# Optimization experiments

Measured on AMD Instinct MI355X. Metric: run time of the kernel, lower is better.

The kernel has to match this reference:

```python
import jax, jax.numpy as jnp
import numpy as np

D_MODEL, N_HEADS, D_HEAD = 1024, 16, 64
BATCH, SEQ = 4, 2048


def setup_inputs() -> dict:
    key = jax.random.key(0)
    ks = jax.random.split(key, 10)
    s = 1.0 / np.sqrt(D_MODEL)
    x = jax.random.normal(ks[0], (BATCH, SEQ, D_MODEL), dtype=jnp.float32)
    attention_mask = jax.random.randint(ks[1], (BATCH, SEQ), 0, 2).astype(jnp.bool_)
    # guarantee at least one attended key per batch row (avoid all -inf softmax)
    attention_mask = attention_mask.at[:, 0].set(True)
    def lin(k):
        kw, kb = jax.random.split(k)
        W = jax.random.uniform(kw, (D_MODEL, D_MODEL), jnp.float32, -s, s)
        b = jax.random.uniform(kb, (D_MODEL,), jnp.float32, -s, s)
        return W, b
    Wq, bq = lin(ks[2]); Wk, bk = lin(ks[3]); Wv, bv = lin(ks[4]); Wo, bo = lin(ks[5])
    return {"x": x, "attention_mask": attention_mask,
            "Wq": Wq, "bq": bq, "Wk": Wk, "bk": bk,
            "Wv": Wv, "bv": bv, "Wo": Wo, "bo": bo}


def reference(x, attention_mask, Wq, bq, Wk, bk, Wv, bv, Wo, bo):
    B, S, _ = x.shape
    def proj(W, b):  # [B,S,d_model] -> [B,S,H,Dh]
        return (x @ W + b).reshape(B, S, N_HEADS, D_HEAD)
    q = proj(Wq, bq)
    k = proj(Wk, bk)
    v = proj(Wv, bv)
    scores = jnp.einsum('bqhd,bkhd->bhqk', q, k)  # [B,H,S,S]
    add_mask = jnp.where(attention_mask, 0.0, jnp.inf)[:, None, None, :]
    # faithful order: subtract mask, THEN scale (inf survives division)
    probs = jax.nn.softmax((scores - add_mask) / jnp.sqrt(jnp.float32(D_HEAD)), axis=-1)
    attn = jnp.einsum('bhqk,bkhd->bqhd', probs, v).reshape(B, S, N_HEADS * D_HEAD)
    return attn @ Wo + bo
```

## Files before the change

kernel.cpp:

```cpp
#include <hip/hip_runtime.h>
#include <hip/hip_bf16.h>
#include <math.h>

#define BATCH 4
#define SEQ   2048
#define DM    1024
#define NH    16
#define DH    64
#define MROWS (BATCH * SEQ)

typedef unsigned short ushort_t;
typedef unsigned int   uint_t;
typedef __attribute__((ext_vector_type(8))) short  short8;
typedef __attribute__((ext_vector_type(4))) float  float4v;

#define QSCALE 0.1803368801111244f

__device__ __forceinline__ ushort_t f2bf(float v) {
    uint_t u = __float_as_uint(v);
    u += 0x7FFFu + ((u >> 16) & 1u);
    return (ushort_t)(u >> 16);
}
__device__ __forceinline__ float bf2f(ushort_t h) {
    return __uint_as_float(((uint_t)h) << 16);
}
__device__ __forceinline__ void gload_lds16(const ushort_t* g, ushort_t* lds) {
    __builtin_amdgcn_global_load_lds(
        (const __attribute__((address_space(1))) void*)g,
        (__attribute__((address_space(3))) void*)lds, 16, 0, 0);
}

__global__ __launch_bounds__(256) void conv_x(
    const float* __restrict__ src, ushort_t* __restrict__ dst, int n4)
{
    int i = blockIdx.x * 256 + threadIdx.x;
    if (i >= n4) return;
    float4 v = ((const float4*)src)[i];
    ((ushort4*)dst)[i] = make_ushort4(f2bf(v.x), f2bf(v.y), f2bf(v.z), f2bf(v.w));
}

__global__ __launch_bounds__(256) void convT_w4(
    const float* __restrict__ W0, const float* __restrict__ W1,
    const float* __restrict__ W2, const float* __restrict__ W3,
    ushort_t* __restrict__ fused, ushort_t* __restrict__ woh,
    ushort_t* __restrict__ wol)
{
    __shared__ float sT[64][65];
    const int z = blockIdx.z;
    const float* W = (z == 0) ? W0 : (z == 1) ? W1 : (z == 2) ? W2 : W3;
    ushort_t* ht = (z < 3) ? fused + (size_t)z * 1024 * 1024 : woh;
    const int n0 = blockIdx.x * 64, k0 = blockIdx.y * 64;
    const int t = threadIdx.x;
#pragma unroll
    for (int i = 0; i < 16; i++) {
        int idx = t + i * 256, r = idx >> 6, c = idx & 63;
        sT[r][c] = W[(size_t)(k0 + r) * 1024 + n0 + c];
    }
    __syncthreads();
#pragma unroll
    for (int i = 0; i < 16; i++) {
        int idx = t + i * 256, r = idx >> 6, c = idx & 63;
        float v = sT[c][r];
        ushort_t h = f2bf(v);
        ht[(size_t)(n0 + r) * 1024 + k0 + c] = h;
        if (z == 3) wol[(size_t)(n0 + r) * 1024 + k0 + c] = f2bf(v - bf2f(h));
    }
}

__global__ __launch_bounds__(256) void gemm_qkv(
    const ushort_t* __restrict__ A, const ushort_t* __restrict__ Bt,
    const float* __restrict__ bq, const float* __restrict__ bk,
    const float* __restrict__ bv, const int* __restrict__ mask,
    ushort_t* __restrict__ Qh, ushort_t* __restrict__ Kh,
    ushort_t* __restrict__ Vt)
{
    __shared__ __align__(16) ushort_t smem[8192];
    const int t = threadIdx.x, lane = t & 63, w = t >> 6;
    const int n0 = blockIdx.x * 128, m0 = blockIdx.y * 128;
    const int wm = (w >> 1) * 64, wn = (w & 1) * 64;
    const int lq = lane >> 4, lc = lane & 15;
    const int gl = (lane & 3) ^ ((lane >> 3) & 3);
    const int irow = lane >> 2;
    const int sect = n0 >> 10;
    const float* bsel = (sect == 0) ? bq : (sect == 1) ? bk : bv;
    const float scl = (sect == 0) ? QSCALE : 1.0f;

    float4v acc[4][4];
#pragma unroll
    for (int i = 0; i < 4; i++)
#pragma unroll
        for (int j = 0; j < 4; j++) acc[i][j] = (float4v)(0.0f);

    for (int k0 = 0; k0 < 1024; k0 += 32) {
        __syncthreads();
#pragma unroll
        for (int j = 0; j < 4; j++) {
            const int i = w * 4 + j;
            const ushort_t* src = (i < 8)
                ? A  + (size_t)(m0 + i * 16 + irow) * 1024 + k0 + gl * 8
                : Bt + (size_t)(n0 + (i - 8) * 16 + irow) * 1024 + k0 + gl * 8;
            gload_lds16(src, &smem[i * 512]);
        }
        __syncthreads();

        short8 av[4], bvf[4];
#pragma unroll
        for (int mt = 0; mt < 4; mt++) {
            const int r = wm + mt * 16 + lc;
            av[mt] = *(const short8*)&smem[r * 32 + ((lq ^ ((r >> 1) & 3)) * 8)];
        }
#pragma unroll
        for (int nt = 0; nt < 4; nt++) {
            const int r = wn + nt * 16 + lc;
            bvf[nt] = *(const short8*)&smem[4096 + r * 32 + ((lq ^ ((r >> 1) & 3)) * 8)];
        }
#pragma unroll
        for (int nt = 0; nt < 4; nt++)
#pragma unroll
            for (int mt = 0; mt < 4; mt++)
                acc[mt][nt] = __builtin_amdgcn_mfma_f32_16x16x32_bf16(av[mt], bvf[nt], acc[mt][nt], 0, 0, 0);
    }

#pragma unroll
    for (int nt = 0; nt < 4; nt++) {
        const int nn = (n0 + wn + nt * 16 + lc) & 1023;
        const float bvv = bsel[nn];
        const int h = nn >> 6, d = nn & 63;
#pragma unroll
        for (int mt = 0; mt < 4; mt++) {
            const int mbase = m0 + wm + mt * 16 + lq * 4;
            const int b = mbase >> 11, s0 = mbase & 2047;
            int mk[4] = {1, 1, 1, 1};
            if (sect != 0) {
                const int4 m4 = *(const int4*)&mask[b * 2048 + s0];
                mk[0] = m4.x; mk[1] = m4.y; mk[2] = m4.z; mk[3] = m4.w;
            }
            if (sect == 2) {
                ushort_t hh[4];
#pragma unroll
                for (int r = 0; r < 4; r++)
                    hh[r] = mk[r] ? f2bf(acc[mt][nt][r] + bvv) : (ushort_t)0;
                *(ushort4*)&Vt[((size_t)(b * 16 + h) * 64 + d) * 2048 + s0] =
                    make_ushort4(hh[0], hh[1], hh[2], hh[3]);
            } else {
                ushort_t* dst = (sect == 0) ? Qh : Kh;
#pragma unroll
                for (int r = 0; r < 4; r++)
                    dst[((size_t)(b * 16 + h) * 2048 + s0 + r) * 64 + d] =
                        mk[r] ? f2bf((acc[mt][nt][r] + bvv) * scl) : (ushort_t)0;
            }
        }
    }
}

__global__ __launch_bounds__(256) void gemm_split3(
    const ushort_t* __restrict__ Ah, const ushort_t* __restrict__ Al,
    const ushort_t* __restrict__ Bh, const ushort_t* __restrict__ Bl,
    const float* __restrict__ bias, float* __restrict__ out)
{
    __shared__ __align__(16) ushort_t smem[16384];
    const int t = threadIdx.x, lane = t & 63, w = t >> 6;
    const int n0 = blockIdx.x * 128, m0 = blockIdx.y * 128;
    const int wm = (w >> 1) * 64, wn = (w & 1) * 64;
    const int lq = lane >> 4, lc = lane & 15;
    const int gl = (lane & 3) ^ ((lane >> 3) & 3);
    const int irow = lane >> 2;

    float4v acc[4][4];
#pragma unroll
    for (int i = 0; i < 4; i++)
#pragma unroll
        for (int j = 0; j < 4; j++) acc[i][j] = (float4v)(0.0f);

    const ushort_t* plane = (w == 0) ? Ah : (w == 1) ? Al : (w == 2) ? Bh : Bl;
    const size_t prow = (size_t)(((w < 2) ? m0 : n0) + irow) * 1024 + gl * 8;

    for (int k0 = 0; k0 < 1024; k0 += 32) {
        __syncthreads();
#pragma unroll
        for (int j = 0; j < 8; j++)
            gload_lds16(plane + prow + (size_t)j * 16384 + k0, &smem[w * 4096 + j * 512]);
        __syncthreads();

        short8 ah[4], al[4];
#pragma unroll
        for (int mt = 0; mt < 4; mt++) {
            const int r = wm + mt * 16 + lc;
            const int off = r * 32 + ((lq ^ ((r >> 1) & 3)) * 8);
            ah[mt] = *(const short8*)&smem[off];
            al[mt] = *(const short8*)&smem[4096 + off];
        }
#pragma unroll
        for (int nt = 0; nt < 4; nt++) {
            const int r = wn + nt * 16 + lc;
            const int off = r * 32 + ((lq ^ ((r >> 1) & 3)) * 8);
            short8 bh = *(const short8*)&smem[8192 + off];
            short8 bl = *(const short8*)&smem[12288 + off];
#pragma unroll
            for (int mt = 0; mt < 4; mt++) {
                acc[mt][nt] = __builtin_amdgcn_mfma_f32_16x16x32_bf16(ah[mt], bh, acc[mt][nt], 0, 0, 0);
                acc[mt][nt] = __builtin_amdgcn_mfma_f32_16x16x32_bf16(al[mt], bh, acc[mt][nt], 0, 0, 0);
                acc[mt][nt] = __builtin_amdgcn_mfma_f32_16x16x32_bf16(ah[mt], bl, acc[mt][nt], 0, 0, 0);
            }
        }
    }

#pragma unroll
    for (int nt = 0; nt < 4; nt++) {
        const int n = n0 + wn + nt * 16 + lc;
        const float bvv = bias[n];
#pragma unroll
        for (int mt = 0; mt < 4; mt++)
#pragma unroll
            for (int r = 0; r < 4; r++) {
                const int m = m0 + wm + mt * 16 + lq * 4 + r;
                out[(size_t)m * 1024 + n] = acc[mt][nt][r] + bvv;
            }
    }
}

__global__ __launch_bounds__(256, 4) void flash_mfma(
    const ushort_t* __restrict__ Q, const ushort_t* __restrict__ K,
    const ushort_t* __restrict__ Vt, const int* __restrict__ mask,
    ushort_t* __restrict__ Oh, ushort_t* __restrict__ Ol)
{
    __shared__ __align__(16) ushort_t smem[16384];
    const int t = threadIdx.x, lane = t & 63, w = t >> 6;
    const int q0 = blockIdx.x * 128;
    const int bh = blockIdx.y, b = bh >> 4, h = bh & 15;
    const int lq = lane >> 4, lc = lane & 15;
    const int wm = w * 32;
    const int gl = (lane & 7) ^ ((lane >> 3) & 7);
    const int lc7 = lc & 7;

    const short8 onesf = (short8)(lc == 0 ? (short)0x3F80 : (short)0);

    int cnt;
    {
        const int4* mrow = (const int4*)(mask + b * SEQ);
        const int4 a = mrow[t * 2], c = mrow[t * 2 + 1];
        cnt = (a.x == 0) + (a.y == 0) + (a.z == 0) + (a.w == 0) +
              (c.x == 0) + (c.y == 0) + (c.z == 0) + (c.w == 0);
#pragma unroll
        for (int off = 1; off < 64; off <<= 1) cnt += __shfl_xor(cnt, off);
        if (lane == 0) ((float*)&smem[8192])[w] = (float)cnt;
    }
#pragma unroll
    for (int j = 0; j < 4; j++) {
        const int i = w * 4 + j;
        gload_lds16(Q + ((size_t)bh * SEQ + q0 + i * 8 + (lane >> 3)) * 64 + gl * 8,
                    &smem[i * 512]);
    }
    __syncthreads();
    const float nmaskf = ((const float*)&smem[8192])[0] + ((const float*)&smem[8192])[1] +
                         ((const float*)&smem[8192])[2] + ((const float*)&smem[8192])[3];

    short8 aq[2][2];
#pragma unroll
    for (int mt = 0; mt < 2; mt++)
#pragma unroll
        for (int kk = 0; kk < 2; kk++) {
            const int r = wm + mt * 16 + lc;
            aq[mt][kk] = *(const short8*)&smem[r * 64 + (((kk * 4 + lq) ^ (r & 7)) * 8)];
        }

    int aK[2], aPw[4], aPr[2];
#pragma unroll
    for (int kk = 0; kk < 2; kk++) {
        aK[kk]  = lc * 64 + (((kk * 4 + lq) ^ lc7) * 8);
        aPr[kk] = wm * 64 + aK[kk];
    }
#pragma unroll
    for (int kt4 = 0; kt4 < 4; kt4++)
        aPw[kt4] = wm * 64 + lc * 64 + (((kt4 * 2 + (lq >> 1)) ^ lc7) * 8) + (lq & 1) * 4;

    const ushort_t* gsrc;
    int gstride;
    int dstbase;
    int jstride;
    if (w < 2) {
        gsrc = K + ((size_t)bh * SEQ + w * 32 + (lane >> 3)) * 64 + gl * 8;
        gstride = 64 * 64;  dstbase = 8192 + w * 2048;  jstride = 512;
    } else {
        gsrc = Vt + ((size_t)bh * 64 + (w - 2) * 32 + (lane >> 3)) * SEQ + gl * 8;
        gstride = 64;       dstbase = 12288 + (w - 2) * 2048;  jstride = 8 * 2048;
    }

    float4v O[2][4];
    float4v lacc[2];
#pragma unroll
    for (int mt = 0; mt < 2; mt++) {
#pragma unroll
        for (int nt = 0; nt < 4; nt++) O[mt][nt] = (float4v)(0.0f);
        lacc[mt] = (float4v)(0.0f);
    }

    for (int kt = 0; kt < 32; kt++) {
        __syncthreads();
#pragma unroll
        for (int j = 0; j < 4; j++)
            gload_lds16(gsrc + j * jstride, &smem[dstbase + j * 512]);
        gsrc += gstride;
        __syncthreads();

        float4v sc[4][2];
#pragma unroll
        for (int kt4 = 0; kt4 < 4; kt4++)
#pragma unroll
            for (int mt = 0; mt < 2; mt++) sc[kt4][mt] = (float4v)(0.0f);
#pragma unroll
        for (int kk = 0; kk < 2; kk++) {
#pragma unroll
            for (int kt4 = 0; kt4 < 4; kt4++) {
                short8 ak = *(const short8*)&smem[8192 + kt4 * 1024 + aK[kk]];
#pragma unroll
                for (int mt = 0; mt < 2; mt++)
                    sc[kt4][mt] = __builtin_amdgcn_mfma_f32_16x16x32_bf16(ak, aq[mt][kk], sc[kt4][mt], 0, 0, 0);
            }
        }

#pragma unroll
        for (int kt4 = 0; kt4 < 4; kt4++) {
#pragma unroll
            for (int mt = 0; mt < 2; mt++) {
                const float p0 = __builtin_amdgcn_exp2f(sc[kt4][mt][0]);
                const float p1 = __builtin_amdgcn_exp2f(sc[kt4][mt][1]);
                const float p2 = __builtin_amdgcn_exp2f(sc[kt4][mt][2]);
                const float p3 = __builtin_amdgcn_exp2f(sc[kt4][mt][3]);
                __hip_bfloat162 pk01 = __float22bfloat162_rn(make_float2(p0, p1));
                __hip_bfloat162 pk23 = __float22bfloat162_rn(make_float2(p2, p3));
                *(uint2*)&smem[mt * 1024 + aPw[kt4]] =
                    make_uint2(*(const uint_t*)&pk01, *(const uint_t*)&pk23);
            }
        }

#pragma unroll
        for (int kk = 0; kk < 2; kk++) {
            short8 ap[2];
#pragma unroll
            for (int mt = 0; mt < 2; mt++)
                ap[mt] = *(const short8*)&smem[mt * 1024 + aPr[kk]];
#pragma unroll
            for (int mt = 0; mt < 2; mt++)
                lacc[mt] = __builtin_amdgcn_mfma_f32_16x16x32_bf16(ap[mt], onesf, lacc[mt], 0, 0, 0);
#pragma unroll
            for (int nt = 0; nt < 4; nt++) {
                short8 bv = *(const short8*)&smem[12288 + nt * 1024 + aK[kk]];
#pragma unroll
                for (int mt = 0; mt < 2; mt++)
                    O[mt][nt] = __builtin_amdgcn_mfma_f32_16x16x32_bf16(ap[mt], bv, O[mt][nt], 0, 0, 0);
            }
        }
    }

#pragma unroll
    for (int mt = 0; mt < 2; mt++) {
#pragma unroll
        for (int r = 0; r < 4; r++) {
            const float lsum = __shfl(lacc[mt][r], lane & 48) - nmaskf;
            const float inv = 1.0f / lsum;
            const int srow = q0 + wm + mt * 16 + lq * 4 + r;
#pragma unroll
            for (int nt = 0; nt < 4; nt++) {
                const float v = O[mt][nt][r] * inv;
                const ushort_t hh = f2bf(v);
                const size_t idx = ((size_t)(b * SEQ + srow)) * 1024 + h * 64 + nt * 16 + lc;
                Oh[idx] = hh;
                Ol[idx] = f2bf(v - bf2f(hh));
            }
        }
    }
}

extern "C" void kernel_launch(void* const* d_in, const int* in_sizes, int n_in,
                              void* d_out, int out_size, void* d_ws, size_t ws_size,
                              hipStream_t stream) {
    const float* x    = (const float*)d_in[0];
    const int*   mask = (const int*)d_in[1];
    const float* Wq   = (const float*)d_in[2];
    const float* bq   = (const float*)d_in[3];
    const float* Wk   = (const float*)d_in[4];
    const float* bk   = (const float*)d_in[5];
    const float* Wv   = (const float*)d_in[6];
    const float* bv   = (const float*)d_in[7];
    const float* Wo   = (const float*)d_in[8];
    const float* bo   = (const float*)d_in[9];
    float* out = (float*)d_out;

    ushort_t* p = (ushort_t*)d_ws;
    const size_t PLANE  = (size_t)MROWS * DM;
    const size_t WPLANE = (size_t)DM * DM;
    ushort_t* xh  = p;  p += PLANE;
    ushort_t* wf  = p;  p += 3 * WPLANE;
    ushort_t* woh = p;  p += WPLANE;
    ushort_t* wol = p;  p += WPLANE;
    ushort_t* Qh  = p;  p += PLANE;
    ushort_t* Kh  = p;  p += PLANE;
    ushort_t* Vth = p;  p += PLANE;
    ushort_t* Ath = p;  p += PLANE;
    ushort_t* Atl = p;  p += PLANE;

    dim3 blk(256);
    hipLaunchKernelGGL(conv_x, dim3(8192), blk, 0, stream, x, xh, 2097152);
    hipLaunchKernelGGL(convT_w4, dim3(16, 16, 4), blk, 0, stream,
                       Wq, Wk, Wv, Wo, wf, woh, wol);
    hipLaunchKernelGGL(gemm_qkv, dim3(24, 64), blk, 0, stream,
                       xh, wf, bq, bk, bv, mask, Qh, Kh, Vth);
    hipLaunchKernelGGL(flash_mfma, dim3(16, 64), blk, 0, stream,
                       Qh, Kh, Vth, mask, Ath, Atl);
    hipLaunchKernelGGL(gemm_split3, dim3(8, 64), blk, 0, stream,
                       Ath, Atl, woh, wol, bo, out);
}
```

Before: 319.4 us.

## Rewrite QKV GEMM as 256x256 double-buffered ping-pong pipeline with block swizzle

Replaces the 128x128 single-buffer QKV projection GEMM with a 256x256 tile computed by 512 threads (8 waves), using a 64-wide K step and a double-buffered 128KB LDS. Global-to-LDS staging for the next K slice is interleaved with MFMA quarters under manual barriers and waitcnts, with s_setprio raising MFMA priority. Block IDs are remapped for better L2 locality. This targets load latency and the sync stalls of the old loop, at the cost of high register pressure, large LDS use and fragile hand-ordered synchronisation.

```diff
diff --git a/kernel.cpp b/kernel.cpp
--- a/kernel.cpp
+++ b/kernel.cpp
@@ -67,68 +67,127 @@
     }
 }
 
-__global__ __launch_bounds__(256) void gemm_qkv(
+#define BAR()   asm volatile("s_barrier" ::: "memory")
+#define LGKM0() asm volatile("s_waitcnt lgkmcnt(0)" ::: "memory")
+#define VMW2()  asm volatile("s_waitcnt vmcnt(2)" ::: "memory")
+
+#define STAGE_A(D, HA, KT) do {                                              \
+    const ushort_t* _s = prowA + (size_t)(HA) * 131072 +                     \
+                         (size_t)((KT) & 15) * 64;                           \
+    gload_lds16(_s,         &smem[(D) * 32768 + (HA) * 8192 + dstw]);        \
+    gload_lds16(_s + 65536, &smem[(D) * 32768 + (HA) * 8192 + 4096 + dstw]); \
+  } while (0)
+
+#define STAGE_B(D, HB, KT) do {                                              \
+    const ushort_t* _s = prowB + (size_t)(HB) * 131072 +                     \
+                         (size_t)((KT) & 15) * 64;                           \
+    gload_lds16(_s,         &smem[(D) * 32768 + 16384 + (HB) * 8192 + dstw]);\
+    gload_lds16(_s + 65536, &smem[(D) * 32768 + 16384 + (HB) * 8192 + 4096 + dstw]); \
+  } while (0)
+
+#define LOAD_A(D, MQ) do {                                                   \
+    const int _b = (D) * 32768 + wm * 8192 + (MQ) * 4096;                    \
+    _Pragma("unroll")                                                        \
+    for (int mf = 0; mf < 4; mf++) {                                         \
+      av[mf][0] = *(const short8*)&smem[_b + mf * 1024 + aA0];               \
+      av[mf][1] = *(const short8*)&smem[_b + mf * 1024 + aA1];               \
+    }                                                                        \
+  } while (0)
+
+#define LOAD_B(D, NQ) do {                                                   \
+    const int _b = (D) * 32768 + 16384 + (wn >> 1) * 8192 +                  \
+                   (wn & 1) * 4096 + (NQ) * 2048;                            \
+    _Pragma("unroll")                                                        \
+    for (int nf = 0; nf < 2; nf++) {                                         \
+      bvf[nf][0] = *(const short8*)&smem[_b + nf * 1024 + aA0];              \
+      bvf[nf][1] = *(const short8*)&smem[_b + nf * 1024 + aA1];              \
+    }                                                                        \
+  } while (0)
+
+#define MFMA_Q(MQ, NQ) do {                                                  \
+    __builtin_amdgcn_s_setprio(1);                                           \
+    _Pragma("unroll")                                                        \
+    for (int kk = 0; kk < 2; kk++)                                           \
+      _Pragma("unroll")                                                      \
+      for (int nf = 0; nf < 2; nf++)                                         \
+        _Pragma("unroll")                                                    \
+        for (int mf = 0; mf < 4; mf++)                                       \
+          acc[(MQ) * 4 + mf][(NQ) * 2 + nf] =                                \
+              __builtin_amdgcn_mfma_f32_16x16x32_bf16(                       \
+                  av[mf][kk], bvf[nf][kk],                                   \
+                  acc[(MQ) * 4 + mf][(NQ) * 2 + nf], 0, 0, 0);               \
+    __builtin_amdgcn_s_setprio(0);                                           \
+  } while (0)
+
+__global__ __launch_bounds__(512, 2) void gemm_qkv(
     const ushort_t* __restrict__ A, const ushort_t* __restrict__ Bt,
     const float* __restrict__ bq, const float* __restrict__ bk,
     const float* __restrict__ bv, const int* __restrict__ mask,
     ushort_t* __restrict__ Qh, ushort_t* __restrict__ Kh,
     ushort_t* __restrict__ Vt)
 {
-    __shared__ __align__(16) ushort_t smem[8192];
+    __shared__ __align__(16) ushort_t smem[65536];
     const int t = threadIdx.x, lane = t & 63, w = t >> 6;
-    const int n0 = blockIdx.x * 128, m0 = blockIdx.y * 128;
-    const int wm = (w >> 1) * 64, wn = (w & 1) * 64;
+
+    int bid = blockIdx.y * 12 + blockIdx.x;
+    bid = (bid & 7) * 48 + (bid >> 3);
+    const int n0 = (bid % 12) * 256, m0 = (bid / 12) * 256;
+
+    const int wm = w >> 2, wn = w & 3;
     const int lq = lane >> 4, lc = lane & 15;
-    const int gl = (lane & 3) ^ ((lane >> 3) & 3);
-    const int irow = lane >> 2;
+    const int gl = (lane & 7) ^ ((lane >> 3) & 7);
     const int sect = n0 >> 10;
     const float* bsel = (sect == 0) ? bq : (sect == 1) ? bk : bv;
     const float scl = (sect == 0) ? QSCALE : 1.0f;
 
-    float4v acc[4][4];
-#pragma unroll
-    for (int i = 0; i < 4; i++)
+    const ushort_t* prowA = A  + (size_t)(m0 + w * 8 + (lane >> 3)) * 1024 + gl * 8;
+    const ushort_t* prowB = Bt + (size_t)(n0 + w * 8 + (lane >> 3)) * 1024 + gl * 8;
+    const int dstw = w * 512;
+
+    const int aA0 = lc * 64 + ((lq ^ (lc & 7)) * 8);
+    const int aA1 = lc * 64 + (((4 + lq) ^ (lc & 7)) * 8);
+
+    float4v acc[8][4];
+#pragma unroll
+    for (int i = 0; i < 8; i++)
 #pragma unroll
         for (int j = 0; j < 4; j++) acc[i][j] = (float4v)(0.0f);
 
-    for (int k0 = 0; k0 < 1024; k0 += 32) {
-        __syncthreads();
-#pragma unroll
-        for (int j = 0; j < 4; j++) {
-            const int i = w * 4 + j;
-            const ushort_t* src = (i < 8)
-                ? A  + (size_t)(m0 + i * 16 + irow) * 1024 + k0 + gl * 8
-                : Bt + (size_t)(n0 + (i - 8) * 16 + irow) * 1024 + k0 + gl * 8;
-            gload_lds16(src, &smem[i * 512]);
-        }
-        __syncthreads();
-
-        short8 av[4], bvf[4];
-#pragma unroll
-        for (int mt = 0; mt < 4; mt++) {
-            const int r = wm + mt * 16 + lc;
-            av[mt] = *(const short8*)&smem[r * 32 + ((lq ^ ((r >> 1) & 3)) * 8)];
-        }
-#pragma unroll
-        for (int nt = 0; nt < 4; nt++) {
-            const int r = wn + nt * 16 + lc;
-            bvf[nt] = *(const short8*)&smem[4096 + r * 32 + ((lq ^ ((r >> 1) & 3)) * 8)];
-        }
-#pragma unroll
-        for (int nt = 0; nt < 4; nt++)
-#pragma unroll
-            for (int mt = 0; mt < 4; mt++)
-                acc[mt][nt] = __builtin_amdgcn_mfma_f32_16x16x32_bf16(av[mt], bvf[nt], acc[mt][nt], 0, 0, 0);
-    }
-
-#pragma unroll
-    for (int nt = 0; nt < 4; nt++) {
-        const int nn = (n0 + wn + nt * 16 + lc) & 1023;
+    short8 av[4][2], bvf[2][2];
+
+    STAGE_A(0, 0, 0); STAGE_B(0, 0, 0); STAGE_A(0, 1, 0); STAGE_B(0, 1, 0);
+    STAGE_A(1, 0, 1);
+    VMW2();
+    BAR();
+
+    for (int i = 0; i < 8; i++) {
+        const int kt = 2 * i;
+        LOAD_A(0, 0); LOAD_B(0, 0); STAGE_A(1, 1, kt + 1);
+        BAR(); LGKM0(); MFMA_Q(0, 0); BAR();
+        LOAD_B(0, 1); STAGE_B(1, 0, kt + 1);
+        BAR(); LGKM0(); MFMA_Q(0, 1); BAR();
+        LOAD_A(0, 1); STAGE_B(1, 1, kt + 1);
+        BAR(); LGKM0(); MFMA_Q(1, 1); BAR();
+        LOAD_B(0, 0); STAGE_A(0, 0, kt + 2);
+        BAR(); LGKM0(); MFMA_Q(1, 0); VMW2(); BAR();
+        LOAD_A(1, 0); LOAD_B(1, 0); STAGE_B(0, 0, kt + 2);
+        BAR(); LGKM0(); MFMA_Q(0, 0); BAR();
+        LOAD_B(1, 1); STAGE_A(0, 1, kt + 2);
+        BAR(); LGKM0(); MFMA_Q(0, 1); BAR();
+        LOAD_A(1, 1); STAGE_B(0, 1, kt + 2);
+        BAR(); LGKM0(); MFMA_Q(1, 1); BAR();
+        LOAD_B(1, 0); STAGE_A(1, 0, kt + 3);
+        BAR(); LGKM0(); MFMA_Q(1, 0); VMW2(); BAR();
+    }
+
+#pragma unroll
+    for (int nf = 0; nf < 4; nf++) {
+        const int nn = (n0 + wn * 64 + nf * 16 + lc) & 1023;
         const float bvv = bsel[nn];
         const int h = nn >> 6, d = nn & 63;
 #pragma unroll
-        for (int mt = 0; mt < 4; mt++) {
-            const int mbase = m0 + wm + mt * 16 + lq * 4;
+        for (int mf = 0; mf < 8; mf++) {
+            const int mbase = m0 + wm * 128 + mf * 16 + lq * 4;
             const int b = mbase >> 11, s0 = mbase & 2047;
             int mk[4] = {1, 1, 1, 1};
             if (sect != 0) {
@@ -139,7 +198,7 @@
                 ushort_t hh[4];
 #pragma unroll
                 for (int r = 0; r < 4; r++)
-                    hh[r] = mk[r] ? f2bf(acc[mt][nt][r] + bvv) : (ushort_t)0;
+                    hh[r] = mk[r] ? f2bf(acc[mf][nf][r] + bvv) : (ushort_t)0;
                 *(ushort4*)&Vt[((size_t)(b * 16 + h) * 64 + d) * 2048 + s0] =
                     make_ushort4(hh[0], hh[1], hh[2], hh[3]);
             } else {
@@ -147,11 +206,20 @@
 #pragma unroll
                 for (int r = 0; r < 4; r++)
                     dst[((size_t)(b * 16 + h) * 2048 + s0 + r) * 64 + d] =
-                        mk[r] ? f2bf((acc[mt][nt][r] + bvv) * scl) : (ushort_t)0;
-            }
-        }
-    }
-}
+                        mk[r] ? f2bf((acc[mf][nf][r] + bvv) * scl) : (ushort_t)0;
+            }
+        }
+    }
+}
+
+#undef STAGE_A
+#undef STAGE_B
+#undef LOAD_A
+#undef LOAD_B
+#undef MFMA_Q
+#undef BAR
+#undef LGKM0
+#undef VMW2
 
 __global__ __launch_bounds__(256) void gemm_split3(
     const ushort_t* __restrict__ Ah, const ushort_t* __restrict__ Al,
@@ -404,7 +472,7 @@
     hipLaunchKernelGGL(conv_x, dim3(8192), blk, 0, stream, x, xh, 2097152);
     hipLaunchKernelGGL(convT_w4, dim3(16, 16, 4), blk, 0, stream,
                        Wq, Wk, Wv, Wo, wf, woh, wol);
-    hipLaunchKernelGGL(gemm_qkv, dim3(24, 64), blk, 0, stream,
+    hipLaunchKernelGGL(gemm_qkv, dim3(12, 32), dim3(512), 0, stream,
                        xh, wf, bq, bk, bv, mask, Qh, Kh, Vth);
     hipLaunchKernelGGL(flash_mfma, dim3(16, 64), blk, 0, stream,
                        Qh, Kh, Vth, mask, Ath, Atl);
```

Result: slower. 331.6 us (+3.8%).
